# Performance work log

Hardware: AMD Instinct MI355X
Metric: run time of the kernel (lower is better)

The kernel has to match this reference:

```python
import jax, jax.numpy as jnp
import numpy as np

NUM_HEADS = 16


def _bayes_w(mu, rho, eps):
    # reparameterized weight sample: w = mu + softplus(rho) * eps
    return mu + jax.nn.softplus(rho) * eps


def setup_inputs() -> dict:
    key = jax.random.key(0)
    ks = jax.random.split(key, 12)
    B, N, C = 4, 2048, 1024
    x = jax.random.normal(ks[0], (B, N, C), jnp.float32)
    w_scale = 0.02
    q_w = jax.random.normal(ks[1], (C, C), jnp.float32) * w_scale
    k_w = jax.random.normal(ks[2], (C, C), jnp.float32) * w_scale
    v_mu = jax.random.normal(ks[3], (C, C), jnp.float32) * w_scale
    v_rho = jax.random.normal(ks[4], (C, C), jnp.float32) * 0.1 - 3.0
    v_eps = jax.random.normal(ks[5], (C, C), jnp.float32)
    proj_mu = jax.random.normal(ks[6], (C, C), jnp.float32) * w_scale
    proj_rho = jax.random.normal(ks[7], (C, C), jnp.float32) * 0.1 - 3.0
    proj_eps = jax.random.normal(ks[8], (C, C), jnp.float32)
    pb_mu = jax.random.normal(ks[9], (C,), jnp.float32) * w_scale
    pb_rho = jax.random.normal(ks[10], (C,), jnp.float32) * 0.1 - 3.0
    pb_eps = jax.random.normal(ks[11], (C,), jnp.float32)
    return {"x": x, "q_w": q_w, "k_w": k_w, "v_mu": v_mu, "v_rho": v_rho,
            "v_eps": v_eps, "proj_mu": proj_mu, "proj_rho": proj_rho,
            "proj_eps": proj_eps, "pb_mu": pb_mu, "pb_rho": pb_rho,
            "pb_eps": pb_eps}


def reference(x, q_w, k_w, v_mu, v_rho, v_eps, proj_mu, proj_rho, proj_eps,
              pb_mu, pb_rho, pb_eps):
    B, N, C = x.shape
    H = NUM_HEADS
    D = C // H
    scale = D ** -0.5
    v_w = _bayes_w(v_mu, v_rho, v_eps)
    # projections (torch Linear: y = x @ W.T)
    q = (x @ q_w.T).reshape(B, N, H, D).transpose(0, 2, 1, 3)  # [B,H,N,D]
    k = (x @ k_w.T).reshape(B, N, H, D).transpose(0, 2, 1, 3)
    v = (x @ v_w.T).reshape(B, N, H, D).transpose(0, 2, 1, 3)
    attn = jax.nn.softmax(jnp.einsum("bhnd,bhmd->bhnm", q * scale, k), axis=-1)
    out = jnp.einsum("bhnm,bhmd->bhnd", attn, v)
    out = out.transpose(0, 2, 1, 3).reshape(B, N, C)
    p_w = _bayes_w(proj_mu, proj_rho, proj_eps)
    p_b = _bayes_w(pb_mu, pb_rho, pb_eps)
    return out @ p_w.T + p_b
```

## Files before the change

kernel.cpp:

```cpp
#include <hip/hip_runtime.h>
#include <hip/hip_bf16.h>
#include <cstdint>
#include <math.h>

typedef __bf16 bf16;
typedef __bf16 bf16x8 __attribute__((ext_vector_type(8)));
typedef __bf16 bf16x4 __attribute__((ext_vector_type(4)));
typedef float  f32x4 __attribute__((ext_vector_type(4)));

#define LOG2E 1.4426950408889634f

#if __has_builtin(__builtin_amdgcn_exp2f)
#define EXP2(x) __builtin_amdgcn_exp2f(x)
#else
#define EXP2(x) exp2f(x)
#endif

#define AS1 __attribute__((address_space(1)))
#define AS3 __attribute__((address_space(3)))

__device__ __forceinline__ void gload_lds16(const bf16* g, bf16* l) {
    __builtin_amdgcn_global_load_lds((AS1 void*)g, (AS3 void*)l, 16, 0, 0);
}

__global__ __launch_bounds__(256)
void cast_f32_bf16(const float* __restrict__ in, bf16* __restrict__ out, int n4) {
    int i = blockIdx.x * 256 + threadIdx.x;
    if (i < n4) {
        float4 v = ((const float4*)in)[i];
        bf16 o[4] = {(bf16)v.x, (bf16)v.y, (bf16)v.z, (bf16)v.w};
        *(uint64_t*)&((bf16*)out)[i * 4] = *(uint64_t*)o;
    }
}

__global__ __launch_bounds__(256)
void bayes_w_kernel(const float* __restrict__ mu, const float* __restrict__ rho,
                    const float* __restrict__ eps, bf16* __restrict__ out, int n) {
    int i = blockIdx.x * 256 + threadIdx.x;
    if (i < n) {
        float r = rho[i];
        float sp = (r > 15.f) ? r : log1pf(expf(r));
        out[i] = (bf16)(mu[i] + sp * eps[i]);
    }
}

__global__ __launch_bounds__(256)
void bayes_b_kernel(const float* __restrict__ mu, const float* __restrict__ rho,
                    const float* __restrict__ eps, float* __restrict__ out, int n) {
    int i = blockIdx.x * 256 + threadIdx.x;
    if (i < n) {
        float r = rho[i];
        float sp = (r > 15.f) ? r : log1pf(expf(r));
        out[i] = mu[i] + sp * eps[i];
    }
}

template <typename OutT>
__global__ __launch_bounds__(256)
void gemm_bt(const bf16* __restrict__ A, const bf16* __restrict__ W,
             OutT* __restrict__ C, const float* __restrict__ bias,
             int M, int N, int K, float q_scale, int q_cols) {
    __shared__ bf16 lA[128 * 32];
    __shared__ bf16 lB[128 * 32];

    const int lane = threadIdx.x & 63;
    const int wv   = threadIdx.x >> 6;
    const int wr   = wv >> 1, wc = wv & 1;

    const int nwg = gridDim.x * gridDim.y;
    int bidl = blockIdx.y * gridDim.x + blockIdx.x;
    if ((nwg & 7) == 0) bidl = (bidl & 7) * (nwg >> 3) + (bidl >> 3);
    const int m0 = (bidl / gridDim.x) * 128, n0 = (bidl % gridDim.x) * 128;

    const int col = lane & 15, quad = lane >> 4;
    const float scale = (n0 < q_cols) ? q_scale : 1.0f;

    const int srow  = wv * 16 + (lane >> 2);
    const int skcol = (lane & 3) * 8;

    f32x4 acc[4][4] = {};

    for (int k0 = 0; k0 < K; k0 += 32) {
#pragma unroll
        for (int r = 0; r < 2; ++r) {
            gload_lds16(A + (size_t)(m0 + r * 64 + srow) * K + k0 + skcol,
                        &lA[(r * 64 + wv * 16) * 32]);
            gload_lds16(W + (size_t)(n0 + r * 64 + srow) * K + k0 + skcol,
                        &lB[(r * 64 + wv * 16) * 32]);
        }
        __syncthreads();

        bf16x8 af[4], bfr[4];
#pragma unroll
        for (int t = 0; t < 4; ++t) {
            af[t]  = *(const bf16x8*)&lA[(wr * 64 + t * 16 + col) * 32 + quad * 8];
            bfr[t] = *(const bf16x8*)&lB[(wc * 64 + t * 16 + col) * 32 + quad * 8];
        }
#pragma unroll
        for (int i = 0; i < 4; ++i)
#pragma unroll
            for (int j = 0; j < 4; ++j)
                acc[i][j] = __builtin_amdgcn_mfma_f32_16x16x32_bf16(af[i], bfr[j], acc[i][j], 0, 0, 0);
        __syncthreads();
    }

#pragma unroll
    for (int i = 0; i < 4; ++i) {
        int row = m0 + wr * 64 + i * 16 + quad * 4;
#pragma unroll
        for (int j = 0; j < 4; ++j) {
            int cc = n0 + wc * 64 + j * 16 + col;
            float bv = bias ? bias[cc] : 0.f;
#pragma unroll
            for (int r = 0; r < 4; ++r)
                C[(size_t)(row + r) * N + cc] = (OutT)(acc[i][j][r] * scale + bv);
        }
    }
}

#define SWZ(row, ec) ((row) * 64 + ((ec) ^ (((row) & 7) << 3)))

__global__ __launch_bounds__(256, 4)
void attn_kernel(const bf16* __restrict__ QKV, bf16* __restrict__ O) {
    __shared__ bf16 sK[2][64 * 64];
    __shared__ bf16 sVt[64 * 64];
    __shared__ bf16 sP [128 * 64];

    const int lane = threadIdx.x & 63;
    const int wv   = threadIdx.x >> 6;
    const int col  = lane & 15, quad = lane >> 4;

    const int bid  = blockIdx.x;
    const int work = (bid & 7) * 128 + (bid >> 3);
    const int qt = work & 15, h = (work >> 4) & 15, b = work >> 8;

    const size_t rowQ0 = (size_t)b * 2048 + qt * 128;
    const bf16* Qg = QKV + rowQ0 * 3072 + h * 64;
    const bf16* Kg = QKV + (size_t)b * 2048 * 3072 + 1024 + h * 64;
    const bf16* Vg = QKV + (size_t)b * 2048 * 3072 + 2048 + h * 64;

    const int rloc = lane >> 3;
    const bf16* Kdma = Kg + (size_t)(wv * 16 + rloc) * 3072 + (((lane & 7) ^ rloc) * 8);

    gload_lds16(Kdma,                    &sK[0][(wv * 16) * 64]);
    gload_lds16(Kdma + (size_t)8 * 3072, &sK[0][(wv * 16 + 8) * 64]);

    const int dc0 = wv * 8, dc1 = 32 + wv * 8;
    bf16x8 vr0 = *(const bf16x8*)&Vg[(size_t)lane * 3072 + dc0];
    bf16x8 vr1 = *(const bf16x8*)&Vg[(size_t)lane * 3072 + dc1];

#pragma unroll
    for (int it = 0; it < 4; ++it) {
        int c = it * 256 + threadIdx.x;
        int row = c >> 3, ec = (c & 7) * 8;
        *(bf16x8*)&sP[SWZ(row, ec)] = *(const bf16x8*)&Qg[(size_t)row * 3072 + ec];
    }
    __syncthreads();
    bf16x8 qf[2][2];
#pragma unroll
    for (int mi = 0; mi < 2; ++mi)
#pragma unroll
        for (int ks = 0; ks < 2; ++ks)
            qf[mi][ks] = *(const bf16x8*)&sP[SWZ(wv * 32 + mi * 16 + col, ks * 32 + quad * 8)];

    f32x4 lsum[2] = {};
    f32x4 o[2][4] = {};
    const int cx = col & 7;

    for (int t = 0; t < 32; ++t) {
        const int p = t & 1;

#pragma unroll
        for (int j = 0; j < 8; ++j) sVt[SWZ(dc0 + j, lane)] = vr0[j];
#pragma unroll
        for (int j = 0; j < 8; ++j) sVt[SWZ(dc1 + j, lane)] = vr1[j];
        __syncthreads();

        if (t < 31) {
            const bf16* kn = Kdma + (size_t)(t * 64 + 64) * 3072;
            gload_lds16(kn,                    &sK[p ^ 1][(wv * 16) * 64]);
            gload_lds16(kn + (size_t)8 * 3072, &sK[p ^ 1][(wv * 16 + 8) * 64]);
        }

        f32x4 st[2][4];
        __builtin_amdgcn_s_setprio(1);
#pragma unroll
        for (int nj = 0; nj < 4; ++nj) {
            bf16x8 kf0 = *(const bf16x8*)&sK[p][(nj * 16 + col) * 64 + ((quad ^ cx) * 8)];
            bf16x8 kf1 = *(const bf16x8*)&sK[p][(nj * 16 + col) * 64 + (((quad ^ cx) ^ 4) * 8)];
#pragma unroll
            for (int mi = 0; mi < 2; ++mi) {
                f32x4 tacc = {0.f, 0.f, 0.f, 0.f};
                tacc = __builtin_amdgcn_mfma_f32_16x16x32_bf16(kf0, qf[mi][0], tacc, 0, 0, 0);
                tacc = __builtin_amdgcn_mfma_f32_16x16x32_bf16(kf1, qf[mi][1], tacc, 0, 0, 0);
                st[mi][nj] = tacc;
            }
        }
        __builtin_amdgcn_s_setprio(0);

#pragma unroll
        for (int mi = 0; mi < 2; ++mi) {
#pragma unroll
            for (int nj = 0; nj < 4; ++nj) {
                f32x4 pv;
#pragma unroll
                for (int r = 0; r < 4; ++r) pv[r] = EXP2(st[mi][nj][r]);
                lsum[mi] += pv;
                bf16x4 pk = {(bf16)pv[0], (bf16)pv[1], (bf16)pv[2], (bf16)pv[3]};
                *(bf16x4*)&sP[SWZ(wv * 32 + mi * 16 + col, nj * 16 + quad * 4)] = pk;
            }
        }

        if (t < 31) {
            const bf16* vn = Vg + (size_t)(t * 64 + 64 + lane) * 3072;
            vr0 = *(const bf16x8*)&vn[dc0];
            vr1 = *(const bf16x8*)&vn[dc1];
        }

        __builtin_amdgcn_s_setprio(1);
#pragma unroll
        for (int ks = 0; ks < 2; ++ks) {
            bf16x8 pf0 = *(const bf16x8*)&sP[SWZ(wv * 32 + col,      ks * 32 + quad * 8)];
            bf16x8 pf1 = *(const bf16x8*)&sP[SWZ(wv * 32 + 16 + col, ks * 32 + quad * 8)];
#pragma unroll
            for (int dj = 0; dj < 4; ++dj) {
                bf16x8 vf = *(const bf16x8*)&sVt[SWZ(dj * 16 + col, ks * 32 + quad * 8)];
                o[0][dj] = __builtin_amdgcn_mfma_f32_16x16x32_bf16(pf0, vf, o[0][dj], 0, 0, 0);
                o[1][dj] = __builtin_amdgcn_mfma_f32_16x16x32_bf16(pf1, vf, o[1][dj], 0, 0, 0);
            }
        }
        __builtin_amdgcn_s_setprio(0);
        __syncthreads();
    }

#pragma unroll
    for (int mi = 0; mi < 2; ++mi) {
        float l = lsum[mi][0] + lsum[mi][1] + lsum[mi][2] + lsum[mi][3];
        l += __shfl_xor(l, 16, 64);
        l += __shfl_xor(l, 32, 64);
#pragma unroll
        for (int r = 0; r < 4; ++r) {
            float inv = 1.f / __shfl(l, quad * 4 + r, 64);
            size_t row = rowQ0 + wv * 32 + mi * 16 + quad * 4 + r;
#pragma unroll
            for (int dj = 0; dj < 4; ++dj)
                O[row * 1024 + h * 64 + dj * 16 + col] = (bf16)(o[mi][dj][r] * inv);
        }
    }
}

extern "C" void kernel_launch(void* const* d_in, const int* in_sizes, int n_in,
                              void* d_out, int out_size, void* d_ws, size_t ws_size,
                              hipStream_t stream) {
    const float* x      = (const float*)d_in[0];
    const float* q_w    = (const float*)d_in[1];
    const float* k_w    = (const float*)d_in[2];
    const float* v_mu   = (const float*)d_in[3];
    const float* v_rho  = (const float*)d_in[4];
    const float* v_eps  = (const float*)d_in[5];
    const float* p_mu   = (const float*)d_in[6];
    const float* p_rho  = (const float*)d_in[7];
    const float* p_eps  = (const float*)d_in[8];
    const float* pb_mu  = (const float*)d_in[9];
    const float* pb_rho = (const float*)d_in[10];
    const float* pb_eps = (const float*)d_in[11];
    float* out = (float*)d_out;

    const size_t MN = (size_t)8192 * 1024;
    const size_t MB = (size_t)1 << 20;
    char* ws = (char*)d_ws;
    bf16*  xb   = (bf16*)(ws);
    bf16*  wqkv = (bf16*)(ws + 16 * MB);
    bf16*  pwb  = (bf16*)(ws + 22 * MB);
    float* p_b  = (float*)(ws + 24 * MB);
    bf16*  QKV  = (bf16*)(ws + 25 * MB);
    bf16*  Ab   = xb;

    const int Wsz = 1024 * 1024;
    cast_f32_bf16<<<(int)(MN / 4 / 256), 256, 0, stream>>>(x, xb, (int)(MN / 4));
    cast_f32_bf16<<<1024, 256, 0, stream>>>(q_w, wqkv, Wsz / 4);
    cast_f32_bf16<<<1024, 256, 0, stream>>>(k_w, wqkv + Wsz, Wsz / 4);
    bayes_w_kernel<<<4096, 256, 0, stream>>>(v_mu, v_rho, v_eps, wqkv + 2 * Wsz, Wsz);
    bayes_w_kernel<<<4096, 256, 0, stream>>>(p_mu, p_rho, p_eps, pwb, Wsz);
    bayes_b_kernel<<<4, 256, 0, stream>>>(pb_mu, pb_rho, pb_eps, p_b, 1024);

    gemm_bt<bf16><<<dim3(24, 64), 256, 0, stream>>>(xb, wqkv, QKV, nullptr,
                                                    8192, 3072, 1024, 0.125f * LOG2E, 1024);

    attn_kernel<<<dim3(1024), 256, 0, stream>>>(QKV, Ab);

    gemm_bt<float><<<dim3(8, 64), 256, 0, stream>>>(Ab, pwb, out, p_b,
                                                    8192, 1024, 1024, 1.0f, 1024);
}
```

Measured before the change: 317.6 us.

## Fuse prep kernels into one launch and double attention query tile per block

Merges the six small cast and Bayesian-weight kernels into a single prep kernel with vectorized float4 loads, cutting launch overhead and scalar memory access. Enlarges the attention query tile from 128 to 256 rows per block, so each wave covers 64 query rows. Each K/V tile loaded into LDS is now reused across twice as many queries. This raises register and LDS use, drops occupancy hints to 2 blocks per CU, and halves the grid to 512 blocks.

```diff
diff --git a/kernel.cpp b/kernel.cpp
--- a/kernel.cpp
+++ b/kernel.cpp
@@ -23,35 +23,60 @@
     __builtin_amdgcn_global_load_lds((AS1 void*)g, (AS3 void*)l, 16, 0, 0);
 }
 
+__device__ __forceinline__ float softplus_f(float r) {
+    return (r > 15.f) ? r : log1pf(expf(r));
+}
+
 __global__ __launch_bounds__(256)
-void cast_f32_bf16(const float* __restrict__ in, bf16* __restrict__ out, int n4) {
-    int i = blockIdx.x * 256 + threadIdx.x;
-    if (i < n4) {
-        float4 v = ((const float4*)in)[i];
+void prep_kernel(const float* __restrict__ x, bf16* __restrict__ xb,
+                 const float* __restrict__ q_w, const float* __restrict__ k_w,
+                 bf16* __restrict__ wqkv,
+                 const float* __restrict__ v_mu, const float* __restrict__ v_rho,
+                 const float* __restrict__ v_eps,
+                 const float* __restrict__ p_mu, const float* __restrict__ p_rho,
+                 const float* __restrict__ p_eps, bf16* __restrict__ pwb,
+                 const float* __restrict__ pb_mu, const float* __restrict__ pb_rho,
+                 const float* __restrict__ pb_eps, float* __restrict__ p_b) {
+    const int Wsz = 1024 * 1024;
+    int blk = blockIdx.x;
+    if (blk < 8192) {
+        int i = blk * 256 + threadIdx.x;
+        float4 v = ((const float4*)x)[i];
         bf16 o[4] = {(bf16)v.x, (bf16)v.y, (bf16)v.z, (bf16)v.w};
-        *(uint64_t*)&((bf16*)out)[i * 4] = *(uint64_t*)o;
-    }
-}
-
-__global__ __launch_bounds__(256)
-void bayes_w_kernel(const float* __restrict__ mu, const float* __restrict__ rho,
-                    const float* __restrict__ eps, bf16* __restrict__ out, int n) {
-    int i = blockIdx.x * 256 + threadIdx.x;
-    if (i < n) {
-        float r = rho[i];
-        float sp = (r > 15.f) ? r : log1pf(expf(r));
-        out[i] = (bf16)(mu[i] + sp * eps[i]);
-    }
-}
-
-__global__ __launch_bounds__(256)
-void bayes_b_kernel(const float* __restrict__ mu, const float* __restrict__ rho,
-                    const float* __restrict__ eps, float* __restrict__ out, int n) {
-    int i = blockIdx.x * 256 + threadIdx.x;
-    if (i < n) {
-        float r = rho[i];
-        float sp = (r > 15.f) ? r : log1pf(expf(r));
-        out[i] = mu[i] + sp * eps[i];
+        *(uint64_t*)&xb[i * 4] = *(uint64_t*)o;
+    } else if (blk < 10240) {
+        const float* src = (blk < 9216) ? q_w : k_w;
+        bf16* dst = (blk < 9216) ? wqkv : wqkv + Wsz;
+        int i = ((blk - 8192) & 1023) * 256 + threadIdx.x;
+        float4 v = ((const float4*)src)[i];
+        bf16 o[4] = {(bf16)v.x, (bf16)v.y, (bf16)v.z, (bf16)v.w};
+        *(uint64_t*)&dst[i * 4] = *(uint64_t*)o;
+    } else if (blk < 12288) {
+        const bool isv = blk < 11264;
+        const float* mu  = isv ? v_mu  : p_mu;
+        const float* rho = isv ? v_rho : p_rho;
+        const float* eps = isv ? v_eps : p_eps;
+        bf16* dst = isv ? wqkv + 2 * Wsz : pwb;
+        int i = ((blk - 10240) & 1023) * 256 + threadIdx.x;
+        float4 m = ((const float4*)mu)[i];
+        float4 r = ((const float4*)rho)[i];
+        float4 e = ((const float4*)eps)[i];
+        bf16 o[4] = {(bf16)(m.x + softplus_f(r.x) * e.x),
+                     (bf16)(m.y + softplus_f(r.y) * e.y),
+                     (bf16)(m.z + softplus_f(r.z) * e.z),
+                     (bf16)(m.w + softplus_f(r.w) * e.w)};
+        *(uint64_t*)&dst[i * 4] = *(uint64_t*)o;
+    } else {
+        int i = threadIdx.x;
+        float4 m = ((const float4*)pb_mu)[i];
+        float4 r = ((const float4*)pb_rho)[i];
+        float4 e = ((const float4*)pb_eps)[i];
+        float4 o;
+        o.x = m.x + softplus_f(r.x) * e.x;
+        o.y = m.y + softplus_f(r.y) * e.y;
+        o.z = m.z + softplus_f(r.z) * e.z;
+        o.w = m.w + softplus_f(r.w) * e.w;
+        ((float4*)p_b)[i] = o;
     }
 }
 
@@ -120,21 +145,21 @@
 
 #define SWZ(row, ec) ((row) * 64 + ((ec) ^ (((row) & 7) << 3)))
 
-__global__ __launch_bounds__(256, 4)
+__global__ __launch_bounds__(256, 2)
 void attn_kernel(const bf16* __restrict__ QKV, bf16* __restrict__ O) {
     __shared__ bf16 sK[2][64 * 64];
     __shared__ bf16 sVt[64 * 64];
-    __shared__ bf16 sP [128 * 64];
+    __shared__ bf16 sP [256 * 64];
 
     const int lane = threadIdx.x & 63;
     const int wv   = threadIdx.x >> 6;
     const int col  = lane & 15, quad = lane >> 4;
 
     const int bid  = blockIdx.x;
-    const int work = (bid & 7) * 128 + (bid >> 3);
-    const int qt = work & 15, h = (work >> 4) & 15, b = work >> 8;
-
-    const size_t rowQ0 = (size_t)b * 2048 + qt * 128;
+    const int work = (bid & 7) * 64 + (bid >> 3);
+    const int qt = work & 7, h = (work >> 3) & 15, b = work >> 7;
+
+    const size_t rowQ0 = (size_t)b * 2048 + qt * 256;
     const bf16* Qg = QKV + rowQ0 * 3072 + h * 64;
     const bf16* Kg = QKV + (size_t)b * 2048 * 3072 + 1024 + h * 64;
     const bf16* Vg = QKV + (size_t)b * 2048 * 3072 + 2048 + h * 64;
@@ -150,21 +175,21 @@
     bf16x8 vr1 = *(const bf16x8*)&Vg[(size_t)lane * 3072 + dc1];
 
 #pragma unroll
-    for (int it = 0; it < 4; ++it) {
+    for (int it = 0; it < 8; ++it) {
         int c = it * 256 + threadIdx.x;
         int row = c >> 3, ec = (c & 7) * 8;
         *(bf16x8*)&sP[SWZ(row, ec)] = *(const bf16x8*)&Qg[(size_t)row * 3072 + ec];
     }
     __syncthreads();
-    bf16x8 qf[2][2];
-#pragma unroll
-    for (int mi = 0; mi < 2; ++mi)
+    bf16x8 qf[4][2];
+#pragma unroll
+    for (int mi = 0; mi < 4; ++mi)
 #pragma unroll
         for (int ks = 0; ks < 2; ++ks)
-            qf[mi][ks] = *(const bf16x8*)&sP[SWZ(wv * 32 + mi * 16 + col, ks * 32 + quad * 8)];
-
-    f32x4 lsum[2] = {};
-    f32x4 o[2][4] = {};
+            qf[mi][ks] = *(const bf16x8*)&sP[SWZ(wv * 64 + mi * 16 + col, ks * 32 + quad * 8)];
+
+    f32x4 lsum[4] = {};
+    f32x4 o[4][4] = {};
     const int cx = col & 7;
 
     for (int t = 0; t < 32; ++t) {
@@ -182,32 +207,33 @@
             gload_lds16(kn + (size_t)8 * 3072, &sK[p ^ 1][(wv * 16 + 8) * 64]);
         }
 
-        f32x4 st[2][4];
-        __builtin_amdgcn_s_setprio(1);
+        bf16x8 kf0[4], kf1[4];
 #pragma unroll
         for (int nj = 0; nj < 4; ++nj) {
-            bf16x8 kf0 = *(const bf16x8*)&sK[p][(nj * 16 + col) * 64 + ((quad ^ cx) * 8)];
-            bf16x8 kf1 = *(const bf16x8*)&sK[p][(nj * 16 + col) * 64 + (((quad ^ cx) ^ 4) * 8)];
-#pragma unroll
-            for (int mi = 0; mi < 2; ++mi) {
+            kf0[nj] = *(const bf16x8*)&sK[p][(nj * 16 + col) * 64 + ((quad ^ cx) * 8)];
+            kf1[nj] = *(const bf16x8*)&sK[p][(nj * 16 + col) * 64 + (((quad ^ cx) ^ 4) * 8)];
+        }
+
+#pragma unroll
+        for (int mi = 0; mi < 4; ++mi) {
+            f32x4 st[4];
+            __builtin_amdgcn_s_setprio(1);
+#pragma unroll
+            for (int nj = 0; nj < 4; ++nj) {
                 f32x4 tacc = {0.f, 0.f, 0.f, 0.f};
-                tacc = __builtin_amdgcn_mfma_f32_16x16x32_bf16(kf0, qf[mi][0], tacc, 0, 0, 0);
-                tacc = __builtin_amdgcn_mfma_f32_16x16x32_bf16(kf1, qf[mi][1], tacc, 0, 0, 0);
-                st[mi][nj] = tacc;
+                tacc = __builtin_amdgcn_mfma_f32_16x16x32_bf16(kf0[nj], qf[mi][0], tacc, 0, 0, 0);
+                tacc = __builtin_amdgcn_mfma_f32_16x16x32_bf16(kf1[nj], qf[mi][1], tacc, 0, 0, 0);
+                st[nj] = tacc;
             }
-        }
-        __builtin_amdgcn_s_setprio(0);
-
-#pragma unroll
-        for (int mi = 0; mi < 2; ++mi) {
+            __builtin_amdgcn_s_setprio(0);
 #pragma unroll
             for (int nj = 0; nj < 4; ++nj) {
                 f32x4 pv;
 #pragma unroll
-                for (int r = 0; r < 4; ++r) pv[r] = EXP2(st[mi][nj][r]);
+                for (int r = 0; r < 4; ++r) pv[r] = EXP2(st[nj][r]);
                 lsum[mi] += pv;
                 bf16x4 pk = {(bf16)pv[0], (bf16)pv[1], (bf16)pv[2], (bf16)pv[3]};
-                *(bf16x4*)&sP[SWZ(wv * 32 + mi * 16 + col, nj * 16 + quad * 4)] = pk;
+                *(bf16x4*)&sP[SWZ(wv * 64 + mi * 16 + col, nj * 16 + quad * 4)] = pk;
             }
         }
 
@@ -220,13 +246,16 @@
         __builtin_amdgcn_s_setprio(1);
 #pragma unroll
         for (int ks = 0; ks < 2; ++ks) {
-            bf16x8 pf0 = *(const bf16x8*)&sP[SWZ(wv * 32 + col,      ks * 32 + quad * 8)];
-            bf16x8 pf1 = *(const bf16x8*)&sP[SWZ(wv * 32 + 16 + col, ks * 32 + quad * 8)];
+            bf16x8 pf[4];
+#pragma unroll
+            for (int mi = 0; mi < 4; ++mi)
+                pf[mi] = *(const bf16x8*)&sP[SWZ(wv * 64 + mi * 16 + col, ks * 32 + quad * 8)];
 #pragma unroll
             for (int dj = 0; dj < 4; ++dj) {
                 bf16x8 vf = *(const bf16x8*)&sVt[SWZ(dj * 16 + col, ks * 32 + quad * 8)];
-                o[0][dj] = __builtin_amdgcn_mfma_f32_16x16x32_bf16(pf0, vf, o[0][dj], 0, 0, 0);
-                o[1][dj] = __builtin_amdgcn_mfma_f32_16x16x32_bf16(pf1, vf, o[1][dj], 0, 0, 0);
+#pragma unroll
+                for (int mi = 0; mi < 4; ++mi)
+                    o[mi][dj] = __builtin_amdgcn_mfma_f32_16x16x32_bf16(pf[mi], vf, o[mi][dj], 0, 0, 0);
             }
         }
         __builtin_amdgcn_s_setprio(0);
@@ -234,14 +263,14 @@
     }
 
 #pragma unroll
-    for (int mi = 0; mi < 2; ++mi) {
+    for (int mi = 0; mi < 4; ++mi) {
         float l = lsum[mi][0] + lsum[mi][1] + lsum[mi][2] + lsum[mi][3];
         l += __shfl_xor(l, 16, 64);
         l += __shfl_xor(l, 32, 64);
 #pragma unroll
         for (int r = 0; r < 4; ++r) {
             float inv = 1.f / __shfl(l, quad * 4 + r, 64);
-            size_t row = rowQ0 + wv * 32 + mi * 16 + quad * 4 + r;
+            size_t row = rowQ0 + wv * 64 + mi * 16 + quad * 4 + r;
 #pragma unroll
             for (int dj = 0; dj < 4; ++dj)
                 O[row * 1024 + h * 64 + dj * 16 + col] = (bf16)(o[mi][dj][r] * inv);
@@ -266,7 +295,6 @@
     const float* pb_eps = (const float*)d_in[11];
     float* out = (float*)d_out;
 
-    const size_t MN = (size_t)8192 * 1024;
     const size_t MB = (size_t)1 << 20;
     char* ws = (char*)d_ws;
     bf16*  xb   = (bf16*)(ws);
@@ -276,18 +304,15 @@
     bf16*  QKV  = (bf16*)(ws + 25 * MB);
     bf16*  Ab   = xb;
 
-    const int Wsz = 1024 * 1024;
-    cast_f32_bf16<<<(int)(MN / 4 / 256), 256, 0, stream>>>(x, xb, (int)(MN / 4));
-    cast_f32_bf16<<<1024, 256, 0, stream>>>(q_w, wqkv, Wsz / 4);
-    cast_f32_bf16<<<1024, 256, 0, stream>>>(k_w, wqkv + Wsz, Wsz / 4);
-    bayes_w_kernel<<<4096, 256, 0, stream>>>(v_mu, v_rho, v_eps, wqkv + 2 * Wsz, Wsz);
-    bayes_w_kernel<<<4096, 256, 0, stream>>>(p_mu, p_rho, p_eps, pwb, Wsz);
-    bayes_b_kernel<<<4, 256, 0, stream>>>(pb_mu, pb_rho, pb_eps, p_b, 1024);
+    prep_kernel<<<12289, 256, 0, stream>>>(x, xb, q_w, k_w, wqkv,
+                                           v_mu, v_rho, v_eps,
+                                           p_mu, p_rho, p_eps, pwb,
+                                           pb_mu, pb_rho, pb_eps, p_b);
 
     gemm_bt<bf16><<<dim3(24, 64), 256, 0, stream>>>(xb, wqkv, QKV, nullptr,
                                                     8192, 3072, 1024, 0.125f * LOG2E, 1024);
 
-    attn_kernel<<<dim3(1024), 256, 0, stream>>>(QKV, Ab);
+    attn_kernel<<<dim3(512), 256, 0, stream>>>(QKV, Ab);
 
     gemm_bt<float><<<dim3(8, 64), 256, 0, stream>>>(Ab, pwb, out, p_b,
                                                     8192, 1024, 1024, 1.0f, 1024);
```

Result: faster. 301.4 us (-5.1%).
